# Kernel optimization log

Hardware: AMD Instinct MI355X
Metric: run time of the kernel (lower is better)

Reference implementation:

```python
import jax, jax.numpy as jnp
import numpy as np
import math

C = 768          # in_channels
KC = 768         # key_channels
VC = 768         # value_channels
H = 12           # head_count
B, N = 8, 2048


def setup_inputs() -> dict:
    key = jax.random.key(0)
    ks = jax.random.split(key, 9)
    s = 0.02
    return {
        "x": jax.random.normal(ks[0], (B, N, C), dtype=jnp.float32),
        # Linear weights stored as (in, out); y = x @ W + b
        "Wq": jax.random.normal(ks[1], (C, KC), dtype=jnp.float32) * s,
        "bq": jnp.zeros((KC,), dtype=jnp.float32),
        "Wk": jax.random.normal(ks[2], (C, KC), dtype=jnp.float32) * s,
        "bk": jnp.zeros((KC,), dtype=jnp.float32),
        "Wv": jax.random.normal(ks[3], (C, VC), dtype=jnp.float32) * s,
        "bv": jnp.zeros((VC,), dtype=jnp.float32),
        "Wr": jax.random.normal(ks[4], (VC, C), dtype=jnp.float32) * s,
        "br": jnp.zeros((C,), dtype=jnp.float32),
    }


def reference(x, Wq, bq, Wk, bk, Wv, bv, Wr, br):
    b, n, c = x.shape
    dk = KC // H  # head key channels
    dv = VC // H  # head value channels
    q = (x @ Wq + bq).reshape(b, n, H, dk)
    k = (x @ Wk + bk).reshape(b, n, H, dk)
    v = (x @ Wv + bv).reshape(b, n, H, dv)
    # NOTE: original scales by sqrt(N) (sequence length), not sqrt(d_head)
    scores = jnp.einsum("bqhd,bkhd->bhqk", q, k) / math.sqrt(n)
    attn = jax.nn.softmax(scores, axis=-1)
    out = jnp.einsum("bhqk,bkhd->bqhd", attn, v).reshape(b, n, VC)
    # reprojection + relu; dropout is identity in eval mode
    return jax.nn.relu(out @ Wr + br)
```

## Files before the change

### kernel.cpp

```cpp
#include <hip/hip_runtime.h>
#include <math.h>

typedef unsigned short u16;
typedef short short8 __attribute__((ext_vector_type(8)));
typedef float f32x4 __attribute__((ext_vector_type(4)));

#define BATCH 8
#define SEQ   2048
#define CH    768
#define NH    12
#define DH    64
#define BH    (BATCH*NH)
#define MTOT  (BATCH*SEQ)

#if __has_builtin(__builtin_amdgcn_exp2f)
#define EXP2F(x) __builtin_amdgcn_exp2f(x)
#else
#define EXP2F(x) exp2f(x)
#endif

#define GL2L(g, l) __builtin_amdgcn_global_load_lds( \
    (const __attribute__((address_space(1))) void*)(g), \
    (__attribute__((address_space(3))) void*)(l), 16, 0, 0)

#define BARRIER_FULL() asm volatile("s_waitcnt vmcnt(0) lgkmcnt(0)\n\ts_barrier" ::: "memory")
#define BARRIER_LDS()  asm volatile("s_waitcnt lgkmcnt(0)\n\ts_barrier" ::: "memory")

#define MFMA16(a, b, c) __builtin_amdgcn_mfma_f32_16x16x32_bf16((a), (b), (c), 0, 0, 0)

__device__ __forceinline__ float bf2f(u16 u) {
  union { unsigned int i; float f; } v; v.i = ((unsigned int)u) << 16; return v.f;
}
__device__ __forceinline__ u16 f2bf(float f) {
  union { float f; unsigned int i; } v; v.f = f;
  return (u16)((v.i + 0x7fffu + ((v.i >> 16) & 1u)) >> 16);
}

__global__ void setup_k(const u16* __restrict__ x, int* __restrict__ flag,
                        const void* b0, const void* b1, const void* b2, const void* b3,
                        u16* __restrict__ biasb) {
  __shared__ int cnt;
  if (threadIdx.x == 0) cnt = 0;
  __syncthreads();
  int big = 0;
  for (int i = 0; i < 8; ++i) {
    u16 u = x[threadIdx.x + i * 256];
    int e = (u >> 7) & 0xFF;
    if (e >= 0x89) big++;
  }
  atomicAdd(&cnt, big);
  __syncthreads();
  int isf = (cnt > 4) ? 1 : 0;
  if (threadIdx.x == 0) *flag = isf;
  for (int t = threadIdx.x; t < 4 * CH; t += 256) {
    int wz = t / CH, c = t - wz * CH;
    const void* src = (wz == 0) ? b0 : (wz == 1) ? b1 : (wz == 2) ? b2 : b3;
    biasb[t] = isf ? f2bf(((const float*)src)[c]) : ((const u16*)src)[c];
  }
}

__global__ __launch_bounds__(256) void cvt_x_k(const void* __restrict__ xin,
                                               u16* __restrict__ xb,
                                               const int* __restrict__ flag) {
  int i4 = (blockIdx.x * 256 + threadIdx.x) * 4;
  if (*flag) {
    float4 f = *(const float4*)((const float*)xin + i4);
    ushort4 o;
    o.x = f2bf(f.x); o.y = f2bf(f.y); o.z = f2bf(f.z); o.w = f2bf(f.w);
    *(ushort4*)(xb + i4) = o;
  } else {
    *(ushort4*)(xb + i4) = *(const ushort4*)((const u16*)xin + i4);
  }
}

__global__ __launch_bounds__(256) void transpose_w4_k(u16* __restrict__ wt,
    const void* w0, const void* w1, const void* w2, const void* w3,
    const int* __restrict__ flag) {
  __shared__ __align__(16) u16 t[64][65];
  const int z = blockIdx.z;
  const void* in = (z == 0) ? w0 : (z == 1) ? w1 : (z == 2) ? w2 : w3;
  u16* out = wt + (size_t)z * CH * CH;
  const int tid = threadIdx.x;
  const int r0 = blockIdx.y * 64, c0 = blockIdx.x * 64;
  const int isf = *flag;
#pragma unroll
  for (int i = 0; i < 16; ++i) {
    int idx = i * 256 + tid;
    int row = idx >> 6, col = idx & 63;
    size_t g = (size_t)(r0 + row) * CH + c0 + col;
    t[row][col] = isf ? f2bf(((const float*)in)[g]) : ((const u16*)in)[g];
  }
  __syncthreads();
#pragma unroll
  for (int i = 0; i < 16; ++i) {
    int idx = i * 256 + tid;
    int orow = idx >> 6, ocol = idx & 63;
    out[(size_t)(c0 + orow) * CH + r0 + ocol] = t[ocol][orow];
  }
}

template <int EPI>
__global__ __launch_bounds__(256) void gemm_bt_k(
    const u16* __restrict__ A, const u16* __restrict__ BtBase,
    const u16* __restrict__ biasb, u16* __restrict__ outBase,
    u16* __restrict__ voutBase, void* __restrict__ finalOut,
    const int* __restrict__ flag, float qscale) {
  const int K = CH;
  const int tid = threadIdx.x;
  const int wv = tid >> 6, lane = tid & 63, quad = lane >> 4, l16 = lane & 15;
  const int wm = (wv >> 1) * 64, wn = (wv & 1) * 64;

  const int id = blockIdx.x;
  const int xcd = id & 7, u = id >> 3;
  int n0, m0, z;
  if (EPI == 0) {
    int n0z = u % 18, yl = u / 18;
    n0 = (n0z % 6) * 128; z = n0z / 6;
    m0 = (xcd + 8 * yl) * 128;
  } else {
    int n0z = u % 6, yl = u / 6;
    n0 = n0z * 128; z = 3;
    m0 = (xcd + 8 * yl) * 128;
  }
  const u16* Bt = BtBase + (size_t)z * CH * CH;
  const u16* bias = biasb + (size_t)z * CH;

  __shared__ __align__(16) u16 As[128 * 64];
  __shared__ __align__(16) u16 Bs[128 * 64];

#define STAGE_AB(kt_) do { \
    _Pragma("unroll") for (int i_ = 0; i_ < 4; ++i_) { \
      int c_ = tid + i_ * 256; \
      int r_ = c_ >> 3; \
      int pg_ = (c_ & 7) ^ (r_ & 7); \
      GL2L(A + (size_t)(m0 + r_) * K + (kt_) + pg_ * 8, As + c_ * 8); \
    } \
    _Pragma("unroll") for (int i_ = 0; i_ < 4; ++i_) { \
      int c_ = tid + i_ * 256; \
      int r_ = c_ >> 3; \
      int pg_ = (c_ & 7) ^ (r_ & 7); \
      GL2L(Bt + (size_t)(n0 + r_) * K + (kt_) + pg_ * 8, Bs + c_ * 8); \
    } } while (0)

  const f32x4 fz4 = {0.f, 0.f, 0.f, 0.f};
  f32x4 acc[4][4];
#pragma unroll
  for (int mt = 0; mt < 4; ++mt)
#pragma unroll
    for (int nt = 0; nt < 4; ++nt) acc[mt][nt] = fz4;

  STAGE_AB(0);

  for (int kt = 0; kt < K; kt += 64) {
    BARRIER_FULL();

    short8 af[4][2], bf[4][2];
#pragma unroll
    for (int mt = 0; mt < 4; ++mt) {
      int r = wm + mt * 16 + l16;
#pragma unroll
      for (int ks = 0; ks < 2; ++ks) {
        int p = (ks * 4 + quad) ^ (r & 7);
        af[mt][ks] = *(const short8*)(As + r * 64 + p * 8);
      }
    }
#pragma unroll
    for (int nt = 0; nt < 4; ++nt) {
      int r = wn + nt * 16 + l16;
#pragma unroll
      for (int ks = 0; ks < 2; ++ks) {
        int p = (ks * 4 + quad) ^ (r & 7);
        bf[nt][ks] = *(const short8*)(Bs + r * 64 + p * 8);
      }
    }
    BARRIER_LDS();
    if (kt + 64 < K) STAGE_AB(kt + 64);

#pragma unroll
    for (int ks = 0; ks < 2; ++ks)
#pragma unroll
      for (int mt = 0; mt < 4; ++mt)
#pragma unroll
        for (int nt = 0; nt < 4; ++nt)
          acc[mt][nt] = __builtin_amdgcn_mfma_f32_16x16x32_bf16(af[mt][ks], bf[nt][ks],
                                                                acc[mt][nt], 0, 0, 0);
  }
#undef STAGE_AB

  const int of32 = (EPI == 1) ? *flag : 0;
#pragma unroll
  for (int mt = 0; mt < 4; ++mt) {
#pragma unroll
    for (int nt = 0; nt < 4; ++nt) {
      int col = n0 + wn + nt * 16 + l16;
      float bv = bf2f(bias[col]);
      int rowb = m0 + wm + mt * 16 + quad * 4;
      if (EPI == 1) {
#pragma unroll
        for (int r = 0; r < 4; ++r) {
          float vv = fmaxf(acc[mt][nt][r] + bv, 0.0f);
          size_t off = (size_t)(rowb + r) * CH + col;
          if (of32) ((float*)finalOut)[off] = vv;
          else      ((u16*)finalOut)[off] = f2bf(vv);
        }
      } else if (z == 2) {
        int b = rowb >> 11, n = rowb & (SEQ - 1);
        int h = col >> 6, d = col & 63;
        int k5 = n & 31;
        int sig = (((k5 & 15) >> 2) << 3) | ((k5 & 16) >> 2);
        int np = (n & ~31) | sig;
        ushort4 pk;
        pk.x = f2bf(acc[mt][nt][0] + bv);
        pk.y = f2bf(acc[mt][nt][1] + bv);
        pk.z = f2bf(acc[mt][nt][2] + bv);
        pk.w = f2bf(acc[mt][nt][3] + bv);
        *(ushort4*)(voutBase + ((size_t)((b * NH + h) * DH + d)) * SEQ + np) = pk;
      } else {
        float sc = (z == 0) ? qscale : 1.0f;
#pragma unroll
        for (int r = 0; r < 4; ++r) {
          float vv = (acc[mt][nt][r] + bv) * sc;
          int row = rowb + r;
          int b = row >> 11, n = row & (SEQ - 1);
          int h = col >> 6, d = col & 63;
          outBase[(size_t)z * BH * SEQ * DH + ((size_t)(b * NH + h) * SEQ + n) * DH + d] = f2bf(vv);
        }
      }
    }
  }
}

__global__ __launch_bounds__(256, 4) void flash_attn_k(
    const u16* __restrict__ Qg, const u16* __restrict__ Kg,
    const u16* __restrict__ Vtg, u16* __restrict__ Og) {
  const int tid = threadIdx.x;
  const int wv = tid >> 6, lane = tid & 63, quad = lane >> 4, l16 = lane & 15;
  const int id = blockIdx.x;
  const int bh = (id & 7) + 8 * (id >> 7);
  const int q0 = ((id >> 3) & 15) * 128;
  const int b = bh / NH, h = bh - b * NH;

  __shared__ __align__(16) u16 smem[16384];

  const f32x4 fz4 = {0.f, 0.f, 0.f, 0.f};
  const short8 ones = {(short)0x3F80, (short)0x3F80, (short)0x3F80, (short)0x3F80,
                       (short)0x3F80, (short)0x3F80, (short)0x3F80, (short)0x3F80};

  const u16* Qp = Qg + (size_t)bh * SEQ * DH + (size_t)q0 * DH;
  const u16* Kp = Kg + (size_t)bh * SEQ * DH;
  const u16* Vp = Vtg + (size_t)bh * DH * SEQ;

#pragma unroll
  for (int i = 0; i < 4; ++i) {
    int c = tid + i * 256; int r = c >> 3; int pg = (c & 7) ^ (r & 7);
    GL2L(Qp + (size_t)r * DH + pg * 8, smem + 8192 + c * 8);
  }
#pragma unroll
  for (int i = 0; i < 2; ++i) {
    int c = tid + i * 256; int r = c >> 3; int pg = (c & 7) ^ (r & 7);
    GL2L(Kp + (size_t)r * DH + pg * 8, smem + c * 8);
    GL2L(Vp + (size_t)r * SEQ + pg * 8, smem + 4096 + c * 8);
  }
  __syncthreads();

  short8 qf[2][2];
#pragma unroll
  for (int mt = 0; mt < 2; ++mt) {
    int r = wv * 32 + mt * 16 + l16;
#pragma unroll
    for (int ks = 0; ks < 2; ++ks) {
      int p = (ks * 4 + quad) ^ (r & 7);
      qf[mt][ks] = *(const short8*)(smem + 8192 + r * 64 + p * 8);
    }
  }

  f32x4 sumacc[2];
  f32x4 oacc[2][4];
  sumacc[0] = fz4; sumacc[1] = fz4;
#pragma unroll
  for (int mt = 0; mt < 2; ++mt)
#pragma unroll
    for (int dt = 0; dt < 4; ++dt) oacc[mt][dt] = fz4;

  int cur = 0;
  for (int k0 = 0; k0 < SEQ; k0 += 64) {
    BARRIER_FULL();
    const u16* Ks = smem + cur * 8192;
    const u16* Vs = Ks + 4096;
    if (k0 + 64 < SEQ) {
      int k1 = k0 + 64;
      u16* Kn = smem + (cur ^ 1) * 8192;
#pragma unroll
      for (int i = 0; i < 2; ++i) {
        int c = tid + i * 256; int r = c >> 3; int pg = (c & 7) ^ (r & 7);
        GL2L(Kp + (size_t)(k1 + r) * DH + pg * 8, Kn + c * 8);
        GL2L(Vp + (size_t)r * SEQ + k1 + pg * 8, Kn + 4096 + c * 8);
      }
    }

    f32x4 s[2][4];
#pragma unroll
    for (int mt = 0; mt < 2; ++mt)
#pragma unroll
      for (int nt = 0; nt < 4; ++nt) s[mt][nt] = fz4;
    __builtin_amdgcn_s_setprio(1);
#pragma unroll
    for (int nt = 0; nt < 4; ++nt) {
      int r = nt * 16 + l16;
#pragma unroll
      for (int ks = 0; ks < 2; ++ks) {
        int p = (ks * 4 + quad) ^ (r & 7);
        short8 kf = *(const short8*)(Ks + r * 64 + p * 8);
        s[0][nt] = __builtin_amdgcn_mfma_f32_16x16x32_bf16(kf, qf[0][ks], s[0][nt], 0, 0, 0);
        s[1][nt] = __builtin_amdgcn_mfma_f32_16x16x32_bf16(kf, qf[1][ks], s[1][nt], 0, 0, 0);
      }
    }
    __builtin_amdgcn_s_setprio(0);

    short8 pf[2][2];
#pragma unroll
    for (int mt = 0; mt < 2; ++mt) {
#pragma unroll
      for (int ks = 0; ks < 2; ++ks) {
        float p0 = EXP2F(s[mt][2 * ks][0]);
        float p1 = EXP2F(s[mt][2 * ks][1]);
        float p2 = EXP2F(s[mt][2 * ks][2]);
        float p3 = EXP2F(s[mt][2 * ks][3]);
        float p4 = EXP2F(s[mt][2 * ks + 1][0]);
        float p5 = EXP2F(s[mt][2 * ks + 1][1]);
        float p6 = EXP2F(s[mt][2 * ks + 1][2]);
        float p7 = EXP2F(s[mt][2 * ks + 1][3]);
        union { unsigned int u[4]; short8 s8; } cv;
        cv.u[0] = __builtin_amdgcn_perm(__float_as_uint(p1), __float_as_uint(p0), 0x07060302u);
        cv.u[1] = __builtin_amdgcn_perm(__float_as_uint(p3), __float_as_uint(p2), 0x07060302u);
        cv.u[2] = __builtin_amdgcn_perm(__float_as_uint(p5), __float_as_uint(p4), 0x07060302u);
        cv.u[3] = __builtin_amdgcn_perm(__float_as_uint(p7), __float_as_uint(p6), 0x07060302u);
        pf[mt][ks] = cv.s8;
      }
    }

    __builtin_amdgcn_s_setprio(1);
    sumacc[0] = MFMA16(pf[0][0], ones, sumacc[0]);
    sumacc[1] = MFMA16(pf[1][0], ones, sumacc[1]);
    sumacc[0] = MFMA16(pf[0][1], ones, sumacc[0]);
    sumacc[1] = MFMA16(pf[1][1], ones, sumacc[1]);
#pragma unroll
    for (int ks = 0; ks < 2; ++ks) {
#pragma unroll
      for (int dt = 0; dt < 4; ++dt) {
        int rv = dt * 16 + l16;
        int p = (ks * 4 + quad) ^ (rv & 7);
        short8 vf = *(const short8*)(Vs + rv * 64 + p * 8);
        oacc[0][dt] = __builtin_amdgcn_mfma_f32_16x16x32_bf16(pf[0][ks], vf, oacc[0][dt], 0, 0, 0);
        oacc[1][dt] = __builtin_amdgcn_mfma_f32_16x16x32_bf16(pf[1][ks], vf, oacc[1][dt], 0, 0, 0);
      }
    }
    __builtin_amdgcn_s_setprio(0);
    cur ^= 1;
  }

#pragma unroll
  for (int mt = 0; mt < 2; ++mt)
#pragma unroll
    for (int r = 0; r < 4; ++r) {
      float inv = 1.0f / sumacc[mt][r];
      int qi = q0 + wv * 32 + mt * 16 + quad * 4 + r;
      size_t base = ((size_t)(b * SEQ) + qi) * CH + h * DH;
#pragma unroll
      for (int dt = 0; dt < 4; ++dt) {
        int d = dt * 16 + l16;
        Og[base + d] = f2bf(oacc[mt][dt][r] * inv);
      }
    }
}

extern "C" void kernel_launch(void* const* d_in, const int* in_sizes, int n_in,
                              void* d_out, int out_size, void* d_ws, size_t ws_size,
                              hipStream_t stream) {
  const void* x  = d_in[0];
  const void* Wq = d_in[1];
  const void* bq = d_in[2];
  const void* Wk = d_in[3];
  const void* bk = d_in[4];
  const void* Wv = d_in[5];
  const void* bv = d_in[6];
  const void* Wr = d_in[7];
  const void* br = d_in[8];
  u16* ws = (u16*)d_ws;

  const size_t WSZ = (size_t)CH * CH;
  const size_t XSZ = (size_t)MTOT * CH;
  int* flag  = (int*)ws;
  u16* biasb = ws + 8;
  u16* wt    = ws + 4096;
  u16* xb    = wt + 4 * WSZ;
  u16* q     = xb + XSZ;
  u16* k     = q + XSZ;
  u16* vt    = k + XSZ;

  const float qscale = (float)(1.4426950408889634 / sqrt(2048.0));

  setup_k<<<1, 256, 0, stream>>>((const u16*)x, flag, bq, bk, bv, br, biasb);
  cvt_x_k<<<XSZ / 1024, 256, 0, stream>>>(x, xb, flag);
  transpose_w4_k<<<dim3(12, 12, 4), 256, 0, stream>>>(wt, Wq, Wk, Wv, Wr, flag);
  gemm_bt_k<0><<<dim3(2304), 256, 0, stream>>>(xb, wt, biasb, q, vt, nullptr,
                                               flag, qscale);
  u16* ao = xb;
  flash_attn_k<<<dim3(1536), 256, 0, stream>>>(q, k, vt, ao);
  gemm_bt_k<1><<<dim3(768), 256, 0, stream>>>(ao, wt, biasb, nullptr, nullptr,
                                              d_out, flag, 1.0f);
}
```

Before: 322.2 us.

## Triple-buffer K/V tiles in flash attention and process two query tiles per block

The attention kernel moves from double to triple buffering of K/V tiles in LDS, prefetching two tiles ahead and waiting with a partial vmcnt so loads overlap more compute. Each block now handles two 128-row query tiles sequentially, which halves the grid to 768 blocks and lowers the occupancy hint from 4 to 3 to fit the larger LDS footprint. The intent is to hide global-load latency behind MFMA work. The risks are lower occupancy and a grid that may not fill all CUs evenly.

```diff
diff --git a/kernel.cpp b/kernel.cpp
--- a/kernel.cpp
+++ b/kernel.cpp
@@ -25,6 +25,7 @@
 
 #define BARRIER_FULL() asm volatile("s_waitcnt vmcnt(0) lgkmcnt(0)\n\ts_barrier" ::: "memory")
 #define BARRIER_LDS()  asm volatile("s_waitcnt lgkmcnt(0)\n\ts_barrier" ::: "memory")
+#define BARRIER_VM4()  asm volatile("s_waitcnt vmcnt(4) lgkmcnt(0)\n\ts_barrier" ::: "memory")
 
 #define MFMA16(a, b, c) __builtin_amdgcn_mfma_f32_16x16x32_bf16((a), (b), (c), 0, 0, 0)
 
@@ -230,148 +231,151 @@
   }
 }
 
-__global__ __launch_bounds__(256, 4) void flash_attn_k(
+__global__ __launch_bounds__(256, 3) void flash_attn_k(
     const u16* __restrict__ Qg, const u16* __restrict__ Kg,
     const u16* __restrict__ Vtg, u16* __restrict__ Og) {
   const int tid = threadIdx.x;
   const int wv = tid >> 6, lane = tid & 63, quad = lane >> 4, l16 = lane & 15;
   const int id = blockIdx.x;
-  const int bh = (id & 7) + 8 * (id >> 7);
-  const int q0 = ((id >> 3) & 15) * 128;
+  const int bh = (id & 7) + 8 * (id >> 6);
+  const int qb = ((id >> 3) & 7) * 128;
   const int b = bh / NH, h = bh - b * NH;
 
-  __shared__ __align__(16) u16 smem[16384];
+  __shared__ __align__(16) u16 smem[24576];
 
   const f32x4 fz4 = {0.f, 0.f, 0.f, 0.f};
   const short8 ones = {(short)0x3F80, (short)0x3F80, (short)0x3F80, (short)0x3F80,
                        (short)0x3F80, (short)0x3F80, (short)0x3F80, (short)0x3F80};
 
-  const u16* Qp = Qg + (size_t)bh * SEQ * DH + (size_t)q0 * DH;
   const u16* Kp = Kg + (size_t)bh * SEQ * DH;
   const u16* Vp = Vtg + (size_t)bh * DH * SEQ;
 
-#pragma unroll
-  for (int i = 0; i < 4; ++i) {
-    int c = tid + i * 256; int r = c >> 3; int pg = (c & 7) ^ (r & 7);
-    GL2L(Qp + (size_t)r * DH + pg * 8, smem + 8192 + c * 8);
-  }
-#pragma unroll
-  for (int i = 0; i < 2; ++i) {
-    int c = tid + i * 256; int r = c >> 3; int pg = (c & 7) ^ (r & 7);
-    GL2L(Kp + (size_t)r * DH + pg * 8, smem + c * 8);
-    GL2L(Vp + (size_t)r * SEQ + pg * 8, smem + 4096 + c * 8);
-  }
-  __syncthreads();
-
-  short8 qf[2][2];
-#pragma unroll
-  for (int mt = 0; mt < 2; ++mt) {
-    int r = wv * 32 + mt * 16 + l16;
-#pragma unroll
-    for (int ks = 0; ks < 2; ++ks) {
-      int p = (ks * 4 + quad) ^ (r & 7);
-      qf[mt][ks] = *(const short8*)(smem + 8192 + r * 64 + p * 8);
-    }
-  }
-
-  f32x4 sumacc[2];
-  f32x4 oacc[2][4];
-  sumacc[0] = fz4; sumacc[1] = fz4;
-#pragma unroll
-  for (int mt = 0; mt < 2; ++mt)
-#pragma unroll
-    for (int dt = 0; dt < 4; ++dt) oacc[mt][dt] = fz4;
-
-  int cur = 0;
-  for (int k0 = 0; k0 < SEQ; k0 += 64) {
-    BARRIER_FULL();
-    const u16* Ks = smem + cur * 8192;
-    const u16* Vs = Ks + 4096;
-    if (k0 + 64 < SEQ) {
-      int k1 = k0 + 64;
-      u16* Kn = smem + (cur ^ 1) * 8192;
-#pragma unroll
-      for (int i = 0; i < 2; ++i) {
-        int c = tid + i * 256; int r = c >> 3; int pg = (c & 7) ^ (r & 7);
-        GL2L(Kp + (size_t)(k1 + r) * DH + pg * 8, Kn + c * 8);
-        GL2L(Vp + (size_t)r * SEQ + k1 + pg * 8, Kn + 4096 + c * 8);
-      }
-    }
-
-    f32x4 s[2][4];
-#pragma unroll
-    for (int mt = 0; mt < 2; ++mt)
-#pragma unroll
-      for (int nt = 0; nt < 4; ++nt) s[mt][nt] = fz4;
-    __builtin_amdgcn_s_setprio(1);
-#pragma unroll
-    for (int nt = 0; nt < 4; ++nt) {
-      int r = nt * 16 + l16;
+#define STAGE_KV(k1, dst) do { \
+    _Pragma("unroll") for (int i_ = 0; i_ < 2; ++i_) { \
+      int c_ = tid + i_ * 256; int r_ = c_ >> 3; int pg_ = (c_ & 7) ^ (r_ & 7); \
+      GL2L(Kp + (size_t)((k1) + r_) * DH + pg_ * 8, (dst) + c_ * 8); \
+      GL2L(Vp + (size_t)r_ * SEQ + (k1) + pg_ * 8, (dst) + 4096 + c_ * 8); \
+    } } while (0)
+
+#define ITER_BODY() do { \
+    f32x4 s[2][4]; \
+    _Pragma("unroll") for (int mt = 0; mt < 2; ++mt) \
+      _Pragma("unroll") for (int nt = 0; nt < 4; ++nt) s[mt][nt] = fz4; \
+    __builtin_amdgcn_s_setprio(1); \
+    _Pragma("unroll") for (int nt = 0; nt < 4; ++nt) { \
+      int r = nt * 16 + l16; \
+      _Pragma("unroll") for (int ks = 0; ks < 2; ++ks) { \
+        int p = (ks * 4 + quad) ^ (r & 7); \
+        short8 kf = *(const short8*)(Ks + r * 64 + p * 8); \
+        s[0][nt] = MFMA16(kf, qf[0][ks], s[0][nt]); \
+        s[1][nt] = MFMA16(kf, qf[1][ks], s[1][nt]); \
+      } \
+    } \
+    __builtin_amdgcn_s_setprio(0); \
+    short8 pf[2][2]; \
+    _Pragma("unroll") for (int mt = 0; mt < 2; ++mt) { \
+      _Pragma("unroll") for (int ks = 0; ks < 2; ++ks) { \
+        float p0 = EXP2F(s[mt][2 * ks][0]); \
+        float p1 = EXP2F(s[mt][2 * ks][1]); \
+        float p2 = EXP2F(s[mt][2 * ks][2]); \
+        float p3 = EXP2F(s[mt][2 * ks][3]); \
+        float p4 = EXP2F(s[mt][2 * ks + 1][0]); \
+        float p5 = EXP2F(s[mt][2 * ks + 1][1]); \
+        float p6 = EXP2F(s[mt][2 * ks + 1][2]); \
+        float p7 = EXP2F(s[mt][2 * ks + 1][3]); \
+        union { unsigned int u[4]; short8 s8; } cv; \
+        cv.u[0] = __builtin_amdgcn_perm(__float_as_uint(p1), __float_as_uint(p0), 0x07060302u); \
+        cv.u[1] = __builtin_amdgcn_perm(__float_as_uint(p3), __float_as_uint(p2), 0x07060302u); \
+        cv.u[2] = __builtin_amdgcn_perm(__float_as_uint(p5), __float_as_uint(p4), 0x07060302u); \
+        cv.u[3] = __builtin_amdgcn_perm(__float_as_uint(p7), __float_as_uint(p6), 0x07060302u); \
+        pf[mt][ks] = cv.s8; \
+      } \
+    } \
+    __builtin_amdgcn_s_setprio(1); \
+    sumacc[0] = MFMA16(pf[0][0], ones, sumacc[0]); \
+    sumacc[1] = MFMA16(pf[1][0], ones, sumacc[1]); \
+    sumacc[0] = MFMA16(pf[0][1], ones, sumacc[0]); \
+    sumacc[1] = MFMA16(pf[1][1], ones, sumacc[1]); \
+    _Pragma("unroll") for (int ks = 0; ks < 2; ++ks) { \
+      _Pragma("unroll") for (int dt = 0; dt < 4; ++dt) { \
+        int rv = dt * 16 + l16; \
+        int p = (ks * 4 + quad) ^ (rv & 7); \
+        short8 vf = *(const short8*)(Vs + rv * 64 + p * 8); \
+        oacc[0][dt] = MFMA16(pf[0][ks], vf, oacc[0][dt]); \
+        oacc[1][dt] = MFMA16(pf[1][ks], vf, oacc[1][dt]); \
+      } \
+    } \
+    __builtin_amdgcn_s_setprio(0); \
+  } while (0)
+
+  for (int qt = 0; qt < 2; ++qt) {
+    const int q0 = qb + qt * 1024;
+    const u16* Qp = Qg + (size_t)bh * SEQ * DH + (size_t)q0 * DH;
+
+#pragma unroll
+    for (int i = 0; i < 4; ++i) {
+      int c = tid + i * 256; int r = c >> 3; int pg = (c & 7) ^ (r & 7);
+      GL2L(Qp + (size_t)r * DH + pg * 8, smem + 16384 + c * 8);
+    }
+    STAGE_KV(0, smem);
+    __syncthreads();
+
+    short8 qf[2][2];
+#pragma unroll
+    for (int mt = 0; mt < 2; ++mt) {
+      int r = wv * 32 + mt * 16 + l16;
 #pragma unroll
       for (int ks = 0; ks < 2; ++ks) {
         int p = (ks * 4 + quad) ^ (r & 7);
-        short8 kf = *(const short8*)(Ks + r * 64 + p * 8);
-        s[0][nt] = __builtin_amdgcn_mfma_f32_16x16x32_bf16(kf, qf[0][ks], s[0][nt], 0, 0, 0);
-        s[1][nt] = __builtin_amdgcn_mfma_f32_16x16x32_bf16(kf, qf[1][ks], s[1][nt], 0, 0, 0);
-      }
-    }
-    __builtin_amdgcn_s_setprio(0);
-
-    short8 pf[2][2];
-#pragma unroll
-    for (int mt = 0; mt < 2; ++mt) {
-#pragma unroll
-      for (int ks = 0; ks < 2; ++ks) {
-        float p0 = EXP2F(s[mt][2 * ks][0]);
-        float p1 = EXP2F(s[mt][2 * ks][1]);
-        float p2 = EXP2F(s[mt][2 * ks][2]);
-        float p3 = EXP2F(s[mt][2 * ks][3]);
-        float p4 = EXP2F(s[mt][2 * ks + 1][0]);
-        float p5 = EXP2F(s[mt][2 * ks + 1][1]);
-        float p6 = EXP2F(s[mt][2 * ks + 1][2]);
-        float p7 = EXP2F(s[mt][2 * ks + 1][3]);
-        union { unsigned int u[4]; short8 s8; } cv;
-        cv.u[0] = __builtin_amdgcn_perm(__float_as_uint(p1), __float_as_uint(p0), 0x07060302u);
-        cv.u[1] = __builtin_amdgcn_perm(__float_as_uint(p3), __float_as_uint(p2), 0x07060302u);
-        cv.u[2] = __builtin_amdgcn_perm(__float_as_uint(p5), __float_as_uint(p4), 0x07060302u);
-        cv.u[3] = __builtin_amdgcn_perm(__float_as_uint(p7), __float_as_uint(p6), 0x07060302u);
-        pf[mt][ks] = cv.s8;
-      }
-    }
-
-    __builtin_amdgcn_s_setprio(1);
-    sumacc[0] = MFMA16(pf[0][0], ones, sumacc[0]);
-    sumacc[1] = MFMA16(pf[1][0], ones, sumacc[1]);
-    sumacc[0] = MFMA16(pf[0][1], ones, sumacc[0]);
-    sumacc[1] = MFMA16(pf[1][1], ones, sumacc[1]);
-#pragma unroll
-    for (int ks = 0; ks < 2; ++ks) {
-#pragma unroll
-      for (int dt = 0; dt < 4; ++dt) {
-        int rv = dt * 16 + l16;
-        int p = (ks * 4 + quad) ^ (rv & 7);
-        short8 vf = *(const short8*)(Vs + rv * 64 + p * 8);
-        oacc[0][dt] = __builtin_amdgcn_mfma_f32_16x16x32_bf16(pf[0][ks], vf, oacc[0][dt], 0, 0, 0);
-        oacc[1][dt] = __builtin_amdgcn_mfma_f32_16x16x32_bf16(pf[1][ks], vf, oacc[1][dt], 0, 0, 0);
-      }
-    }
-    __builtin_amdgcn_s_setprio(0);
-    cur ^= 1;
-  }
-
-#pragma unroll
-  for (int mt = 0; mt < 2; ++mt)
-#pragma unroll
-    for (int r = 0; r < 4; ++r) {
-      float inv = 1.0f / sumacc[mt][r];
-      int qi = q0 + wv * 32 + mt * 16 + quad * 4 + r;
-      size_t base = ((size_t)(b * SEQ) + qi) * CH + h * DH;
-#pragma unroll
-      for (int dt = 0; dt < 4; ++dt) {
-        int d = dt * 16 + l16;
-        Og[base + d] = f2bf(oacc[mt][dt][r] * inv);
-      }
-    }
+        qf[mt][ks] = *(const short8*)(smem + 16384 + r * 64 + p * 8);
+      }
+    }
+    BARRIER_LDS();
+    STAGE_KV(64, smem + 8192);
+
+    f32x4 sumacc[2];
+    f32x4 oacc[2][4];
+    sumacc[0] = fz4; sumacc[1] = fz4;
+#pragma unroll
+    for (int mt = 0; mt < 2; ++mt)
+#pragma unroll
+      for (int dt = 0; dt < 4; ++dt) oacc[mt][dt] = fz4;
+
+    int cur = 0;
+    for (int t = 0; t < 31; ++t) {
+      BARRIER_VM4();
+      const u16* Ks = smem + cur * 8192;
+      const u16* Vs = Ks + 4096;
+      if (t < 30) {
+        int b2 = cur - 1; if (b2 < 0) b2 += 3;
+        STAGE_KV((t + 2) * 64, smem + b2 * 8192);
+      }
+      ITER_BODY();
+      cur = (cur == 2) ? 0 : cur + 1;
+    }
+    BARRIER_FULL();
+    {
+      const u16* Ks = smem + cur * 8192;
+      const u16* Vs = Ks + 4096;
+      ITER_BODY();
+    }
+
+#pragma unroll
+    for (int mt = 0; mt < 2; ++mt)
+#pragma unroll
+      for (int r = 0; r < 4; ++r) {
+        float inv = 1.0f / sumacc[mt][r];
+        int qi = q0 + wv * 32 + mt * 16 + quad * 4 + r;
+        size_t base = ((size_t)(b * SEQ) + qi) * CH + h * DH;
+#pragma unroll
+        for (int dt = 0; dt < 4; ++dt) {
+          int d = dt * 16 + l16;
+          Og[base + d] = f2bf(oacc[mt][dt][r] * inv);
+        }
+      }
+  }
+#undef ITER_BODY
+#undef STAGE_KV
 }
 
 extern "C" void kernel_launch(void* const* d_in, const int* in_sizes, int n_in,
@@ -406,7 +410,7 @@
   gemm_bt_k<0><<<dim3(2304), 256, 0, stream>>>(xb, wt, biasb, q, vt, nullptr,
                                                flag, qscale);
   u16* ao = xb;
-  flash_attn_k<<<dim3(1536), 256, 0, stream>>>(q, k, vt, ao);
+  flash_attn_k<<<dim3(768), 256, 0, stream>>>(q, k, vt, ao);
   gemm_bt_k<1><<<dim3(768), 256, 0, stream>>>(ao, wt, biasb, nullptr, nullptr,
                                               d_out, flag, 1.0f);
 }
```

Measured after the change: 340.8 us. 5.8% more time.

## Double-buffer LDS tiles in projection GEMM to overlap loads with MFMA

Applied to the files above, without the earlier changes.

Replaces the single-buffer GEMM main loop with a ping-pong pair of A/B LDS buffers, so the next K-tile is fetched with global_load_lds while MFMAs run on the current one. This drops the extra LDS-only barrier per iteration. It also adds a min-blocks hint of 2 to launch_bounds. LDS use doubles to 64 KB per block, which can lower occupancy, and the loop is manually unrolled by two K-tiles.

```diff
diff --git a/kernel.cpp b/kernel.cpp
--- a/kernel.cpp
+++ b/kernel.cpp
@@ -24,7 +24,6 @@
     (__attribute__((address_space(3))) void*)(l), 16, 0, 0)
 
 #define BARRIER_FULL() asm volatile("s_waitcnt vmcnt(0) lgkmcnt(0)\n\ts_barrier" ::: "memory")
-#define BARRIER_LDS()  asm volatile("s_waitcnt lgkmcnt(0)\n\ts_barrier" ::: "memory")
 
 #define MFMA16(a, b, c) __builtin_amdgcn_mfma_f32_16x16x32_bf16((a), (b), (c), 0, 0, 0)
 
@@ -100,7 +99,7 @@
 }
 
 template <int EPI>
-__global__ __launch_bounds__(256) void gemm_bt_k(
+__global__ __launch_bounds__(256, 2) void gemm_bt_k(
     const u16* __restrict__ A, const u16* __restrict__ BtBase,
     const u16* __restrict__ biasb, u16* __restrict__ outBase,
     u16* __restrict__ voutBase, void* __restrict__ finalOut,
@@ -125,22 +124,47 @@
   const u16* Bt = BtBase + (size_t)z * CH * CH;
   const u16* bias = biasb + (size_t)z * CH;
 
-  __shared__ __align__(16) u16 As[128 * 64];
-  __shared__ __align__(16) u16 Bs[128 * 64];
-
-#define STAGE_AB(kt_) do { \
+  __shared__ __align__(16) u16 smem[32768];
+  u16* const As0 = smem;
+  u16* const Bs0 = smem + 8192;
+  u16* const As1 = smem + 16384;
+  u16* const Bs1 = smem + 24576;
+
+#define STAGE_AB(kt_, AsD, BsD) do { \
     _Pragma("unroll") for (int i_ = 0; i_ < 4; ++i_) { \
       int c_ = tid + i_ * 256; \
       int r_ = c_ >> 3; \
       int pg_ = (c_ & 7) ^ (r_ & 7); \
-      GL2L(A + (size_t)(m0 + r_) * K + (kt_) + pg_ * 8, As + c_ * 8); \
+      GL2L(A + (size_t)(m0 + r_) * K + (kt_) + pg_ * 8, (AsD) + c_ * 8); \
     } \
     _Pragma("unroll") for (int i_ = 0; i_ < 4; ++i_) { \
       int c_ = tid + i_ * 256; \
       int r_ = c_ >> 3; \
       int pg_ = (c_ & 7) ^ (r_ & 7); \
-      GL2L(Bt + (size_t)(n0 + r_) * K + (kt_) + pg_ * 8, Bs + c_ * 8); \
+      GL2L(Bt + (size_t)(n0 + r_) * K + (kt_) + pg_ * 8, (BsD) + c_ * 8); \
     } } while (0)
+
+#define COMPUTE_TILE(AsS, BsS) do { \
+    short8 af[4][2], bf[4][2]; \
+    _Pragma("unroll") for (int mt = 0; mt < 4; ++mt) { \
+      int r = wm + mt * 16 + l16; \
+      _Pragma("unroll") for (int ks = 0; ks < 2; ++ks) { \
+        int p = (ks * 4 + quad) ^ (r & 7); \
+        af[mt][ks] = *(const short8*)((AsS) + r * 64 + p * 8); \
+      } \
+    } \
+    _Pragma("unroll") for (int nt = 0; nt < 4; ++nt) { \
+      int r = wn + nt * 16 + l16; \
+      _Pragma("unroll") for (int ks = 0; ks < 2; ++ks) { \
+        int p = (ks * 4 + quad) ^ (r & 7); \
+        bf[nt][ks] = *(const short8*)((BsS) + r * 64 + p * 8); \
+      } \
+    } \
+    _Pragma("unroll") for (int ks = 0; ks < 2; ++ks) \
+      _Pragma("unroll") for (int mt = 0; mt < 4; ++mt) \
+        _Pragma("unroll") for (int nt = 0; nt < 4; ++nt) \
+          acc[mt][nt] = MFMA16(af[mt][ks], bf[nt][ks], acc[mt][nt]); \
+  } while (0)
 
   const f32x4 fz4 = {0.f, 0.f, 0.f, 0.f};
   f32x4 acc[4][4];
@@ -149,43 +173,18 @@
 #pragma unroll
     for (int nt = 0; nt < 4; ++nt) acc[mt][nt] = fz4;
 
-  STAGE_AB(0);
-
-  for (int kt = 0; kt < K; kt += 64) {
+  STAGE_AB(0, As0, Bs0);
+
+  for (int kp = 0; kp < K; kp += 128) {
     BARRIER_FULL();
-
-    short8 af[4][2], bf[4][2];
-#pragma unroll
-    for (int mt = 0; mt < 4; ++mt) {
-      int r = wm + mt * 16 + l16;
-#pragma unroll
-      for (int ks = 0; ks < 2; ++ks) {
-        int p = (ks * 4 + quad) ^ (r & 7);
-        af[mt][ks] = *(const short8*)(As + r * 64 + p * 8);
-      }
-    }
-#pragma unroll
-    for (int nt = 0; nt < 4; ++nt) {
-      int r = wn + nt * 16 + l16;
-#pragma unroll
-      for (int ks = 0; ks < 2; ++ks) {
-        int p = (ks * 4 + quad) ^ (r & 7);
-        bf[nt][ks] = *(const short8*)(Bs + r * 64 + p * 8);
-      }
-    }
-    BARRIER_LDS();
-    if (kt + 64 < K) STAGE_AB(kt + 64);
-
-#pragma unroll
-    for (int ks = 0; ks < 2; ++ks)
-#pragma unroll
-      for (int mt = 0; mt < 4; ++mt)
-#pragma unroll
-        for (int nt = 0; nt < 4; ++nt)
-          acc[mt][nt] = __builtin_amdgcn_mfma_f32_16x16x32_bf16(af[mt][ks], bf[nt][ks],
-                                                                acc[mt][nt], 0, 0, 0);
+    if (kp + 64 < K) STAGE_AB(kp + 64, As1, Bs1);
+    COMPUTE_TILE(As0, Bs0);
+    BARRIER_FULL();
+    if (kp + 128 < K) STAGE_AB(kp + 128, As0, Bs0);
+    COMPUTE_TILE(As1, Bs1);
   }
 #undef STAGE_AB
+#undef COMPUTE_TILE
 
   const int of32 = (EPI == 1) ? *flag : 0;
 #pragma unroll
```

Result: slower. 333.6 us (+3.5%).
